# Performance work log

Measured on AMD Instinct MI355X. Metric: run time of the kernel, lower is better.

The kernel has to match this reference:

```python
import math
import jax, jax.numpy as jnp
import numpy as np

H, D_H = 16, 128  # heads, head_dim; d = H*D_H = 2048

def _heads_view(w, rank):
    # w: (d, r) -> (H, r, d_h), matching torch view(H, d_h, r).transpose(1, 2)
    return jnp.transpose(w.reshape(H, D_H, rank), (0, 2, 1))

def setup_inputs() -> dict:
    key = jax.random.key(0)
    ks = jax.random.split(key, 9)
    d, rq, rk, rv = 2048, 512, 512, 512
    B, T = 2, 2048
    s = 0.02  # GPT-2 style init scale keeps logits numerically sane
    return {
        "x": jax.random.normal(ks[0], (B, T, d), dtype=jnp.float32),
        "q_down_w": jax.random.normal(ks[1], (rq, d), dtype=jnp.float32) * s,
        "k_down_w": jax.random.normal(ks[2], (rk, d), dtype=jnp.float32) * s,
        "v_down_w": jax.random.normal(ks[3], (rv, d), dtype=jnp.float32) * s,
        "q_up_w": jax.random.normal(ks[4], (d, rq), dtype=jnp.float32) * s,
        "k_up_w": jax.random.normal(ks[5], (d, rk), dtype=jnp.float32) * s,
        "v_up_w": jax.random.normal(ks[6], (d, rv), dtype=jnp.float32) * s,
        "out_w": jax.random.normal(ks[7], (d, d), dtype=jnp.float32) * s,
        "out_b": jnp.zeros((d,), dtype=jnp.float32),
    }

def reference(x, q_down_w, k_down_w, v_down_w, q_up_w, k_up_w, v_up_w, out_w, out_b):
    B, T, d = x.shape
    rq, rk, rv = q_down_w.shape[0], k_down_w.shape[0], v_down_w.shape[0]
    # Down projections (nn.Linear: x @ W^T)
    Qd = x @ q_down_w.T            # [B, T, rq]
    Kd = x @ k_down_w.T            # [B, S, rk] (S == T, no past_kv)
    Vd = x @ v_down_w.T            # [B, S, rv]
    S = Kd.shape[1]
    # Absorbed score matrix M: [H, rq, rk]
    Uq_h = _heads_view(q_up_w, rq)  # [H, rq, d_h]
    Uk_h = _heads_view(k_up_w, rk)  # [H, rk, d_h]
    M = jnp.einsum('hqd,hkd->hqk', Uq_h, Uk_h) * (1.0 / math.sqrt(D_H))
    # Logits via factorized path: [B,H,T,rk] then [B,H,T,S]
    Qm = jnp.einsum('btq,hqk->bhtk', Qd, M)
    logits = jnp.einsum('bhtk,bsk->bhts', Qm, Kd)
    # Causal mask (P = S - T = 0)
    P = S - T
    i = jnp.arange(T)[:, None]
    j = jnp.arange(S)[None, :]
    future = j > (P + i)
    logits = jnp.where(future[None, None], -jnp.inf, logits)
    attn = jax.nn.softmax(logits.astype(jnp.float32), axis=-1)
    attn = jnp.nan_to_num(attn).astype(x.dtype)
    # Values path
    Uv_h = _heads_view(v_up_w, rv)                      # [H, rv, d_h]
    V_up = jnp.einsum('bsr,hrd->bhsd', Vd, Uv_h)        # [B, H, S, d_h]
    ctx = jnp.einsum('bhts,bhsd->bhtd', attn, V_up)     # [B, H, T, d_h]
    ctx = jnp.transpose(ctx, (0, 2, 1, 3)).reshape(B, T, d)
    out = ctx @ out_w.T + out_b
    return out
```

## Files before the change

### kernel.cpp

```cpp
#include <hip/hip_runtime.h>
#include <stdint.h>

typedef __bf16 bf16x8 __attribute__((ext_vector_type(8)));
typedef float  f32x4  __attribute__((ext_vector_type(4)));
typedef float  f32x16 __attribute__((ext_vector_type(16)));
typedef unsigned short u16;
typedef unsigned int u32;
typedef u16 u16x8 __attribute__((ext_vector_type(8)));
typedef u32 u32x4 __attribute__((ext_vector_type(4)));

__device__ __forceinline__ u16 f2bf(float f) {
  uint32_t u = __builtin_bit_cast(uint32_t, f);
  u += 0x7fffu + ((u >> 16) & 1u);
  return (u16)(u >> 16);
}
__device__ __forceinline__ u32 pack2(float lo, float hi) {
  return (u32)f2bf(lo) | ((u32)f2bf(hi) << 16);
}

__device__ __forceinline__ void async_cp16(const void* src, void* lds) {
  __builtin_amdgcn_global_load_lds(
      (const __attribute__((address_space(1))) uint32_t*)src,
      (__attribute__((address_space(3))) uint32_t*)lds, 16, 0, 0);
}

struct CvtArgs {
  const float* in[8];
  u16* out[8];
  int n8[8];
  int nblk[8];
};
__global__ void cvt_multi(CvtArgs a) {
  int bx = blockIdx.x;
  int t = 0;
  while (t < 7 && bx >= a.nblk[t]) { bx -= a.nblk[t]; ++t; }
  const int i = bx * 256 + threadIdx.x;
  if (i >= a.n8[t]) return;
  const float4* p = (const float4*)a.in[t] + (size_t)i * 2;
  float4 va = p[0], vb = p[1];
  u16x8 r;
  r[0] = f2bf(va.x); r[1] = f2bf(va.y); r[2] = f2bf(va.z); r[3] = f2bf(va.w);
  r[4] = f2bf(vb.x); r[5] = f2bf(vb.y); r[6] = f2bf(vb.z); r[7] = f2bf(vb.w);
  ((u16x8*)a.out[t])[i] = r;
}

struct GemmB3 {
  const u16* A[3];
  const u16* Bm[3];
  u16* C[3];
  float alpha[3];
};

template<bool F32OUT>
__global__ __launch_bounds__(256, 2)
void gemm_bt(GemmB3 args, float* __restrict__ Cf, const float* __restrict__ bias,
             int M, int N, int K)
{
  __shared__ u16 At[128 * 32];
  __shared__ u16 Bt[128 * 32];
  const int z = blockIdx.z;
  const u16* __restrict__ A  = args.A[z];
  const u16* __restrict__ Bw = args.Bm[z];
  const int bm = blockIdx.x * 128;
  const int bn = blockIdx.y * 128;
  const int tid = threadIdx.x;
  const int w  = tid >> 6;
  const int l  = tid & 63;
  const int lr = l & 15;
  const int lg = l >> 4;
  const int wr = (w >> 1) * 64;
  const int wc = (w & 1) * 64;

  f32x4 acc[4][4];
  #pragma unroll
  for (int m = 0; m < 4; ++m)
    #pragma unroll
    for (int n = 0; n < 4; ++n) acc[m][n] = (f32x4){0.f, 0.f, 0.f, 0.f};

  for (int k0 = 0; k0 < K; k0 += 32) {
    __syncthreads();
    #pragma unroll
    for (int i = 0; i < 2; ++i) {
      const int gidx = i * 256 + tid;
      const int row  = gidx >> 2;
      const int g    = gidx & 3;
      const int gs   = (g - (row >> 1)) & 3;
      async_cp16(A  + (size_t)(bm + row) * K + k0 + gs * 8,
                 At + (size_t)(i * 256 + w * 64) * 8);
      async_cp16(Bw + (size_t)(bn + row) * K + k0 + gs * 8,
                 Bt + (size_t)(i * 256 + w * 64) * 8);
    }
    __syncthreads();
    bf16x8 af[4], bfr[4];
    #pragma unroll
    for (int m = 0; m < 4; ++m) {
      const int row = wr + m * 16 + lr;
      const int pos = (lg + (row >> 1)) & 3;
      af[m] = *(const bf16x8*)(At + row * 32 + pos * 8);
    }
    #pragma unroll
    for (int n = 0; n < 4; ++n) {
      const int row = wc + n * 16 + lr;
      const int pos = (lg + (row >> 1)) & 3;
      bfr[n] = *(const bf16x8*)(Bt + row * 32 + pos * 8);
    }
    #pragma unroll
    for (int m = 0; m < 4; ++m)
      #pragma unroll
      for (int n = 0; n < 4; ++n)
        acc[m][n] = __builtin_amdgcn_mfma_f32_16x16x32_bf16(af[m], bfr[n], acc[m][n], 0, 0, 0);
  }

  if constexpr (F32OUT) {
    #pragma unroll
    for (int n = 0; n < 4; ++n) {
      const int col = bn + wc + n * 16 + lr;
      const float bv = bias[col];
      #pragma unroll
      for (int m = 0; m < 4; ++m) {
        const int rbase = bm + wr + m * 16 + lg * 4;
        #pragma unroll
        for (int j = 0; j < 4; ++j)
          Cf[(size_t)(rbase + j) * N + col] = acc[m][n][j] + bv;
      }
    }
  } else {
    u16* __restrict__ C = args.C[z];
    const float alpha = args.alpha[z];
    #pragma unroll
    for (int n = 0; n < 4; ++n) {
      const int col = bn + wc + n * 16 + lr;
      #pragma unroll
      for (int m = 0; m < 4; ++m) {
        const int rbase = bm + wr + m * 16 + lg * 4;
        #pragma unroll
        for (int j = 0; j < 4; ++j)
          C[(size_t)(rbase + j) * N + col] = f2bf(acc[m][n][j] * alpha);
      }
    }
  }
}

__global__ __launch_bounds__(256, 2)
void mla_attn(const u16* __restrict__ Qu, const u16* __restrict__ Ku,
              const u16* __restrict__ Vtg, u16* __restrict__ ctx)
{
  __shared__ u16 Ktb[2][64 * 128];
  __shared__ u16 Vtb[2][128 * 64];

  const int bid = blockIdx.x;
  const int kk  = bid >> 5;
  const int qt  = (kk & 1) ? (kk >> 1) : (15 - (kk >> 1));
  const int bh  = bid & 31;
  const int b = bh >> 4, h = bh & 15;
  const int qbase = qt * 128;
  const int tid = threadIdx.x;
  const int w = tid >> 6, l = tid & 63;
  const int ql = l & 31;
  const int hi = l >> 5;
  const bool hb = (hi != 0);
  const int T = 2048;
  const size_t rs = 2048;

  const u16* Qp = Qu + ((size_t)b * T) * rs + (size_t)h * 128;
  const u16* Kp = Ku + ((size_t)b * T) * rs + (size_t)h * 128;
  const u16* Vp = Vtg + (size_t)(h * 128) * 4096 + (size_t)b * T;

  const int qw = qbase + w * 32;
  const int qg = qw + ql;

  bf16x8 qf[8];
  #pragma unroll
  for (int kb = 0; kb < 8; ++kb)
    qf[kb] = *(const bf16x8*)(Qp + (size_t)qg * rs + kb * 16 + hi * 8);

  f32x16 acc[4];
  #pragma unroll
  for (int dt = 0; dt < 4; ++dt)
    #pragma unroll
    for (int r = 0; r < 16; ++r) acc[dt][r] = 0.f;
  float mrun = -1.0e30f, lsum = 0.f;

  const int ksr = tid >> 4;
  const u16* kb0 = Kp + (size_t)ksr * rs + (((tid & 15) ^ (ksr & 15)) * 8);
  const int vsr = tid >> 3;
  const u16* vb0 = Vp + (size_t)vsr * 4096 + (((tid & 7) ^ (vsr & 7)) * 8);

  const int nT = 2 * qt + 2;

  auto stage = [&](int buf, int it) {
    const int s0 = it * 64;
    #pragma unroll
    for (int i = 0; i < 4; ++i)
      async_cp16(kb0 + (size_t)(s0 + i * 16) * rs, &Ktb[buf][(i * 256 + w * 64) * 8]);
    #pragma unroll
    for (int i = 0; i < 4; ++i)
      async_cp16(vb0 + (size_t)(i * 32) * 4096 + s0, &Vtb[buf][(i * 256 + w * 64) * 8]);
  };

  stage(0, 0);
  int cur = 0;

  for (int it = 0; it < nT; ++it) {
    __syncthreads();
    if (it + 1 < nT) stage(cur ^ 1, it + 1);
    const int s0 = it * 64;
    if (s0 <= qw + 31) {
      const u16* Kt = Ktb[cur];
      const u16* Vt = Vtb[cur];
      const bool diag = (it == (qw >> 6));
      #pragma unroll
      for (int st = 0; st < 2; ++st) {
        f32x16 c;
        #pragma unroll
        for (int r = 0; r < 16; ++r) c[r] = 0.f;
        __builtin_amdgcn_s_setprio(1);
        #pragma unroll
        for (int kb = 0; kb < 8; ++kb) {
          bf16x8 kf = *(const bf16x8*)(Kt + (st * 32 + ql) * 128 +
                                       (((2 * kb + hi) ^ (ql & 15)) * 8));
          c = __builtin_amdgcn_mfma_f32_32x32x16_bf16(kf, qf[kb], c, 0, 0, 0);
        }
        __builtin_amdgcn_s_setprio(0);

        float p[16];
        if (diag) {
          #pragma unroll
          for (int r = 0; r < 16; ++r) {
            const int sgl = s0 + st * 32 + 4 * hi + (r & 3) + 8 * (r >> 2);
            p[r] = (sgl <= qg) ? c[r] : -INFINITY;
          }
        } else {
          #pragma unroll
          for (int r = 0; r < 16; ++r) p[r] = c[r];
        }
        float mx = p[0];
        #pragma unroll
        for (int r = 1; r < 16; ++r) mx = fmaxf(mx, p[r]);
        mx = fmaxf(mx, __shfl_xor(mx, 32));
        if (__any(mx > mrun + 8.f)) {
          const float mnew = fmaxf(mrun, mx);
          const float scl = exp2f(mrun - mnew);
          mrun = mnew;
          lsum *= scl;
          #pragma unroll
          for (int dt = 0; dt < 4; ++dt)
            #pragma unroll
            for (int r = 0; r < 16; ++r) acc[dt][r] *= scl;
        }
        float psum = 0.f;
        #pragma unroll
        for (int r = 0; r < 16; ++r) { p[r] = exp2f(p[r] - mrun); psum += p[r]; }
        lsum += psum + __shfl_xor(psum, 32);

        u32 P0 = pack2(p[0], p[1]),   P1 = pack2(p[2], p[3]);
        u32 P2 = pack2(p[4], p[5]),   P3 = pack2(p[6], p[7]);
        u32 P4 = pack2(p[8], p[9]),   P5 = pack2(p[10], p[11]);
        u32 P6 = pack2(p[12], p[13]), P7 = pack2(p[14], p[15]);
        u32 X0 = __shfl_xor(P0, 32), X1 = __shfl_xor(P1, 32);
        u32 X2 = __shfl_xor(P2, 32), X3 = __shfl_xor(P3, 32);
        u32 X4 = __shfl_xor(P4, 32), X5 = __shfl_xor(P5, 32);
        u32 X6 = __shfl_xor(P6, 32), X7 = __shfl_xor(P7, 32);
        const bf16x8 f0 = __builtin_bit_cast(bf16x8,
            (u32x4){hb ? X2 : P0, hb ? X3 : P1, hb ? P2 : X0, hb ? P3 : X1});
        const bf16x8 f1 = __builtin_bit_cast(bf16x8,
            (u32x4){hb ? X6 : P4, hb ? X7 : P5, hb ? P6 : X4, hb ? P7 : X5});

        __builtin_amdgcn_s_setprio(1);
        #pragma unroll
        for (int dt = 0; dt < 4; ++dt) {
          const int vrow = (dt * 32 + ql) * 64;
          bf16x8 v0 = *(const bf16x8*)(Vt + vrow + (((2 * (2 * st)     + hi) ^ (ql & 7)) * 8));
          bf16x8 v1 = *(const bf16x8*)(Vt + vrow + (((2 * (2 * st + 1) + hi) ^ (ql & 7)) * 8));
          acc[dt] = __builtin_amdgcn_mfma_f32_32x32x16_bf16(v0, f0, acc[dt], 0, 0, 0);
          acc[dt] = __builtin_amdgcn_mfma_f32_32x32x16_bf16(v1, f1, acc[dt], 0, 0, 0);
        }
        __builtin_amdgcn_s_setprio(0);
      }
    }
    cur ^= 1;
  }

  __syncthreads();
  u16* Ot = &Ktb[0][0];
  const float inv = 1.f / lsum;
  const int orow = w * 32 + ql;
  #pragma unroll
  for (int dt = 0; dt < 4; ++dt) {
    #pragma unroll
    for (int rq = 0; rq < 4; ++rq) {
      const int dhb = dt * 32 + 8 * rq + 4 * hi;
      const int dhs = dhb ^ ((ql & 15) << 3);
      u16 e0 = f2bf(acc[dt][rq * 4 + 0] * inv);
      u16 e1 = f2bf(acc[dt][rq * 4 + 1] * inv);
      u16 e2 = f2bf(acc[dt][rq * 4 + 2] * inv);
      u16 e3 = f2bf(acc[dt][rq * 4 + 3] * inv);
      u32 w0 = (u32)e0 | ((u32)e1 << 16);
      u32 w1 = (u32)e2 | ((u32)e3 << 16);
      *(u32*)(Ot + orow * 128 + dhs)     = w0;
      *(u32*)(Ot + orow * 128 + dhs + 2) = w1;
    }
  }
  __syncthreads();
  #pragma unroll
  for (int i = 0; i < 8; ++i) {
    const int n = i * 256 + tid;
    const int q = n >> 4, g = n & 15;
    bf16x8 v = *(const bf16x8*)(Ot + q * 128 + ((g ^ (q & 15)) * 8));
    *(bf16x8*)(ctx + ((size_t)b * T + qbase + q) * rs + h * 128 + g * 8) = v;
  }
}

extern "C" void kernel_launch(void* const* d_in, const int* in_sizes, int n_in,
                              void* d_out, int out_size, void* d_ws, size_t ws_size,
                              hipStream_t stream)
{
  (void)n_in; (void)out_size; (void)ws_size;
  const float* x   = (const float*)d_in[0];
  const float* qdw = (const float*)d_in[1];
  const float* kdw = (const float*)d_in[2];
  const float* vdw = (const float*)d_in[3];
  const float* quw = (const float*)d_in[4];
  const float* kuw = (const float*)d_in[5];
  const float* vuw = (const float*)d_in[6];
  const float* oww = (const float*)d_in[7];
  const float* ob  = (const float*)d_in[8];

  const int d = 2048, r = 512;
  const int BT = in_sizes[0] / d;

  u16* p = (u16*)d_ws;
  auto take = [&](size_t n) { u16* q = p; p += n; return q; };
  u16* xb  = take((size_t)BT * d);
  u16* wqd = take((size_t)r * d);
  u16* wkd = take((size_t)r * d);
  u16* wvd = take((size_t)r * d);
  u16* wqu = take((size_t)d * r);
  u16* wku = take((size_t)d * r);
  u16* wvu = take((size_t)d * r);
  u16* wow = take((size_t)d * d);
  u16* Qd  = take((size_t)BT * r);
  u16* Kd  = take((size_t)BT * r);
  u16* Vd  = take((size_t)BT * r);
  u16* Qu  = take((size_t)BT * d);
  u16* Ku  = take((size_t)BT * d);
  u16* Vtg = take((size_t)BT * d);
  u16* ctx = take((size_t)BT * d);

  CvtArgs ca;
  const float* ins[8] = {x, oww, qdw, kdw, vdw, quw, kuw, vuw};
  u16* outs[8]        = {xb, wow, wqd, wkd, wvd, wqu, wku, wvu};
  const size_t ns[8]  = {(size_t)BT * d, (size_t)d * d,
                         (size_t)r * d, (size_t)r * d, (size_t)r * d,
                         (size_t)d * r, (size_t)d * r, (size_t)d * r};
  int total_blk = 0;
  for (int t = 0; t < 8; ++t) {
    ca.in[t] = ins[t]; ca.out[t] = outs[t];
    ca.n8[t] = (int)(ns[t] / 8);
    ca.nblk[t] = (ca.n8[t] + 255) / 256;
    total_blk += ca.nblk[t];
  }
  cvt_multi<<<dim3(total_blk), dim3(256), 0, stream>>>(ca);

  GemmB3 g1;
  g1.A[0] = xb;  g1.A[1] = xb;  g1.A[2] = xb;
  g1.Bm[0] = wqd; g1.Bm[1] = wkd; g1.Bm[2] = wvd;
  g1.C[0] = Qd;  g1.C[1] = Kd;  g1.C[2] = Vd;
  g1.alpha[0] = 1.f; g1.alpha[1] = 1.f; g1.alpha[2] = 1.f;
  gemm_bt<false><<<dim3(BT / 128, r / 128, 3), dim3(256), 0, stream>>>(
      g1, nullptr, nullptr, BT, r, d);

  GemmB3 g2;
  g2.A[0] = Qd;  g2.A[1] = Kd;  g2.A[2] = Kd;
  g2.Bm[0] = wqu; g2.Bm[1] = wku; g2.Bm[2] = wku;
  g2.C[0] = Qu;  g2.C[1] = Ku;  g2.C[2] = Ku;
  g2.alpha[0] = 0.12751743f; g2.alpha[1] = 1.f; g2.alpha[2] = 1.f;
  gemm_bt<false><<<dim3(BT / 128, d / 128, 2), dim3(256), 0, stream>>>(
      g2, nullptr, nullptr, BT, d, r);

  GemmB3 g2v;
  g2v.A[0] = wvu; g2v.A[1] = wvu; g2v.A[2] = wvu;
  g2v.Bm[0] = Vd; g2v.Bm[1] = Vd; g2v.Bm[2] = Vd;
  g2v.C[0] = Vtg; g2v.C[1] = Vtg; g2v.C[2] = Vtg;
  g2v.alpha[0] = 1.f; g2v.alpha[1] = 1.f; g2v.alpha[2] = 1.f;
  gemm_bt<false><<<dim3(d / 128, BT / 128, 1), dim3(256), 0, stream>>>(
      g2v, nullptr, nullptr, d, BT, r);

  mla_attn<<<dim3(512), dim3(256), 0, stream>>>(Qu, Ku, Vtg, ctx);

  GemmB3 g3;
  g3.A[0] = ctx; g3.A[1] = ctx; g3.A[2] = ctx;
  g3.Bm[0] = wow; g3.Bm[1] = wow; g3.Bm[2] = wow;
  g3.C[0] = nullptr; g3.C[1] = nullptr; g3.C[2] = nullptr;
  g3.alpha[0] = 1.f; g3.alpha[1] = 1.f; g3.alpha[2] = 1.f;
  gemm_bt<true><<<dim3(BT / 128, d / 128, 1), dim3(256), 0, stream>>>(
      g3, (float*)d_out, ob, BT, d, d);
}
```

Before: 239.1 us.

## Widen GEMM K-tile, merge attention sub-tiles, use hardware bf16 pack

The GEMM kernel now stages a 64-wide K slice per barrier pair instead of 32, using an XOR swizzle over 8 groups, which halves the number of sync points. The attention inner loop computes both 32-key score blocks before running a single softmax over all 64 keys, so the max, rescale and sum steps run once per tile instead of twice. Packing to bf16 now uses the v_cvt_pk_bf16_f32 instruction instead of manual rounding. The cross-half exchange is cut from 8 shuffles per sub-tile to 4 by selecting the needed word before the shuffle. The cost is more LDS per GEMM block and more live registers in the attention loop.

```diff
diff --git a/kernel.cpp b/kernel.cpp
--- a/kernel.cpp
+++ b/kernel.cpp
@@ -14,8 +14,10 @@
   u += 0x7fffu + ((u >> 16) & 1u);
   return (u16)(u >> 16);
 }
-__device__ __forceinline__ u32 pack2(float lo, float hi) {
-  return (u32)f2bf(lo) | ((u32)f2bf(hi) << 16);
+__device__ __forceinline__ u32 cvtpk(float lo, float hi) {
+  u32 r;
+  asm("v_cvt_pk_bf16_f32 %0, %1, %2" : "=v"(r) : "v"(lo), "v"(hi));
+  return r;
 }
 
 __device__ __forceinline__ void async_cp16(const void* src, void* lds) {
@@ -56,8 +58,8 @@
 void gemm_bt(GemmB3 args, float* __restrict__ Cf, const float* __restrict__ bias,
              int M, int N, int K)
 {
-  __shared__ u16 At[128 * 32];
-  __shared__ u16 Bt[128 * 32];
+  __shared__ u16 At[128 * 64];
+  __shared__ u16 Bt[128 * 64];
   const int z = blockIdx.z;
   const u16* __restrict__ A  = args.A[z];
   const u16* __restrict__ Bw = args.Bm[z];
@@ -77,38 +79,41 @@
     #pragma unroll
     for (int n = 0; n < 4; ++n) acc[m][n] = (f32x4){0.f, 0.f, 0.f, 0.f};
 
-  for (int k0 = 0; k0 < K; k0 += 32) {
+  for (int k0 = 0; k0 < K; k0 += 64) {
     __syncthreads();
     #pragma unroll
-    for (int i = 0; i < 2; ++i) {
-      const int gidx = i * 256 + tid;
-      const int row  = gidx >> 2;
-      const int g    = gidx & 3;
-      const int gs   = (g - (row >> 1)) & 3;
+    for (int i = 0; i < 4; ++i) {
+      const int slot = i * 256 + tid;
+      const int row  = slot >> 3;
+      const int pos  = slot & 7;
+      const int gs   = pos ^ (row & 7);
       async_cp16(A  + (size_t)(bm + row) * K + k0 + gs * 8,
                  At + (size_t)(i * 256 + w * 64) * 8);
       async_cp16(Bw + (size_t)(bn + row) * K + k0 + gs * 8,
                  Bt + (size_t)(i * 256 + w * 64) * 8);
     }
     __syncthreads();
-    bf16x8 af[4], bfr[4];
-    #pragma unroll
-    for (int m = 0; m < 4; ++m) {
-      const int row = wr + m * 16 + lr;
-      const int pos = (lg + (row >> 1)) & 3;
-      af[m] = *(const bf16x8*)(At + row * 32 + pos * 8);
-    }
-    #pragma unroll
-    for (int n = 0; n < 4; ++n) {
-      const int row = wc + n * 16 + lr;
-      const int pos = (lg + (row >> 1)) & 3;
-      bfr[n] = *(const bf16x8*)(Bt + row * 32 + pos * 8);
-    }
-    #pragma unroll
-    for (int m = 0; m < 4; ++m)
-      #pragma unroll
-      for (int n = 0; n < 4; ++n)
-        acc[m][n] = __builtin_amdgcn_mfma_f32_16x16x32_bf16(af[m], bfr[n], acc[m][n], 0, 0, 0);
+    #pragma unroll
+    for (int kk = 0; kk < 2; ++kk) {
+      bf16x8 af[4], bfr[4];
+      #pragma unroll
+      for (int m = 0; m < 4; ++m) {
+        const int row = wr + m * 16 + lr;
+        const int pos = (kk * 4 + lg) ^ (row & 7);
+        af[m] = *(const bf16x8*)(At + row * 64 + pos * 8);
+      }
+      #pragma unroll
+      for (int n = 0; n < 4; ++n) {
+        const int row = wc + n * 16 + lr;
+        const int pos = (kk * 4 + lg) ^ (row & 7);
+        bfr[n] = *(const bf16x8*)(Bt + row * 64 + pos * 8);
+      }
+      #pragma unroll
+      for (int m = 0; m < 4; ++m)
+        #pragma unroll
+        for (int n = 0; n < 4; ++n)
+          acc[m][n] = __builtin_amdgcn_mfma_f32_16x16x32_bf16(af[m], bfr[n], acc[m][n], 0, 0, 0);
+    }
   }
 
   if constexpr (F32OUT) {
@@ -209,74 +214,83 @@
       const u16* Kt = Ktb[cur];
       const u16* Vt = Vtb[cur];
       const bool diag = (it == (qw >> 6));
+
+      f32x16 c0, c1;
+      #pragma unroll
+      for (int r = 0; r < 16; ++r) { c0[r] = 0.f; c1[r] = 0.f; }
+      __builtin_amdgcn_s_setprio(1);
+      #pragma unroll
+      for (int kb = 0; kb < 8; ++kb) {
+        bf16x8 kf0 = *(const bf16x8*)(Kt + ql * 128 + (((2 * kb + hi) ^ (ql & 15)) * 8));
+        c0 = __builtin_amdgcn_mfma_f32_32x32x16_bf16(kf0, qf[kb], c0, 0, 0, 0);
+      }
+      #pragma unroll
+      for (int kb = 0; kb < 8; ++kb) {
+        bf16x8 kf1 = *(const bf16x8*)(Kt + (32 + ql) * 128 + (((2 * kb + hi) ^ (ql & 15)) * 8));
+        c1 = __builtin_amdgcn_mfma_f32_32x32x16_bf16(kf1, qf[kb], c1, 0, 0, 0);
+      }
+      __builtin_amdgcn_s_setprio(0);
+
+      float p[32];
+      if (diag) {
+        #pragma unroll
+        for (int r = 0; r < 16; ++r) {
+          const int sg0 = s0 + 4 * hi + (r & 3) + 8 * (r >> 2);
+          p[r]      = (sg0      <= qg) ? c0[r] : -INFINITY;
+          p[16 + r] = (sg0 + 32 <= qg) ? c1[r] : -INFINITY;
+        }
+      } else {
+        #pragma unroll
+        for (int r = 0; r < 16; ++r) { p[r] = c0[r]; p[16 + r] = c1[r]; }
+      }
+      float mx = fmaxf(p[0], p[1]);
+      #pragma unroll
+      for (int r = 2; r < 32; ++r) mx = fmaxf(mx, p[r]);
+      mx = fmaxf(mx, __shfl_xor(mx, 32));
+      if (__any(mx > mrun + 8.f)) {
+        const float mnew = fmaxf(mrun, mx);
+        const float scl = exp2f(mrun - mnew);
+        mrun = mnew;
+        lsum *= scl;
+        #pragma unroll
+        for (int dt = 0; dt < 4; ++dt)
+          #pragma unroll
+          for (int r = 0; r < 16; ++r) acc[dt][r] *= scl;
+      }
+      float psum = 0.f;
+      #pragma unroll
+      for (int r = 0; r < 32; ++r) { p[r] = exp2f(p[r] - mrun); psum += p[r]; }
+      lsum += psum + __shfl_xor(psum, 32);
+
+      bf16x8 fr[4];
       #pragma unroll
       for (int st = 0; st < 2; ++st) {
-        f32x16 c;
-        #pragma unroll
-        for (int r = 0; r < 16; ++r) c[r] = 0.f;
-        __builtin_amdgcn_s_setprio(1);
-        #pragma unroll
-        for (int kb = 0; kb < 8; ++kb) {
-          bf16x8 kf = *(const bf16x8*)(Kt + (st * 32 + ql) * 128 +
-                                       (((2 * kb + hi) ^ (ql & 15)) * 8));
-          c = __builtin_amdgcn_mfma_f32_32x32x16_bf16(kf, qf[kb], c, 0, 0, 0);
+        const int o = st * 16;
+        u32 P0 = cvtpk(p[o + 0], p[o + 1]),   P1 = cvtpk(p[o + 2], p[o + 3]);
+        u32 P2 = cvtpk(p[o + 4], p[o + 5]),   P3 = cvtpk(p[o + 6], p[o + 7]);
+        u32 P4 = cvtpk(p[o + 8], p[o + 9]),   P5 = cvtpk(p[o + 10], p[o + 11]);
+        u32 P6 = cvtpk(p[o + 12], p[o + 13]), P7 = cvtpk(p[o + 14], p[o + 15]);
+        u32 Y0 = __shfl_xor(hb ? P0 : P2, 32);
+        u32 Y1 = __shfl_xor(hb ? P1 : P3, 32);
+        u32 Y2 = __shfl_xor(hb ? P4 : P6, 32);
+        u32 Y3 = __shfl_xor(hb ? P5 : P7, 32);
+        fr[st * 2 + 0] = __builtin_bit_cast(bf16x8,
+            (u32x4){hb ? Y0 : P0, hb ? Y1 : P1, hb ? P2 : Y0, hb ? P3 : Y1});
+        fr[st * 2 + 1] = __builtin_bit_cast(bf16x8,
+            (u32x4){hb ? Y2 : P4, hb ? Y3 : P5, hb ? P6 : Y2, hb ? P7 : Y3});
+      }
+
+      __builtin_amdgcn_s_setprio(1);
+      #pragma unroll
+      for (int dt = 0; dt < 4; ++dt) {
+        const int vrow = (dt * 32 + ql) * 64;
+        #pragma unroll
+        for (int ks = 0; ks < 4; ++ks) {
+          bf16x8 v = *(const bf16x8*)(Vt + vrow + (((2 * ks + hi) ^ (ql & 7)) * 8));
+          acc[dt] = __builtin_amdgcn_mfma_f32_32x32x16_bf16(v, fr[ks], acc[dt], 0, 0, 0);
         }
-        __builtin_amdgcn_s_setprio(0);
-
-        float p[16];
-        if (diag) {
-          #pragma unroll
-          for (int r = 0; r < 16; ++r) {
-            const int sgl = s0 + st * 32 + 4 * hi + (r & 3) + 8 * (r >> 2);
-            p[r] = (sgl <= qg) ? c[r] : -INFINITY;
-          }
-        } else {
-          #pragma unroll
-          for (int r = 0; r < 16; ++r) p[r] = c[r];
-        }
-        float mx = p[0];
-        #pragma unroll
-        for (int r = 1; r < 16; ++r) mx = fmaxf(mx, p[r]);
-        mx = fmaxf(mx, __shfl_xor(mx, 32));
-        if (__any(mx > mrun + 8.f)) {
-          const float mnew = fmaxf(mrun, mx);
-          const float scl = exp2f(mrun - mnew);
-          mrun = mnew;
-          lsum *= scl;
-          #pragma unroll
-          for (int dt = 0; dt < 4; ++dt)
-            #pragma unroll
-            for (int r = 0; r < 16; ++r) acc[dt][r] *= scl;
-        }
-        float psum = 0.f;
-        #pragma unroll
-        for (int r = 0; r < 16; ++r) { p[r] = exp2f(p[r] - mrun); psum += p[r]; }
-        lsum += psum + __shfl_xor(psum, 32);
-
-        u32 P0 = pack2(p[0], p[1]),   P1 = pack2(p[2], p[3]);
-        u32 P2 = pack2(p[4], p[5]),   P3 = pack2(p[6], p[7]);
-        u32 P4 = pack2(p[8], p[9]),   P5 = pack2(p[10], p[11]);
-        u32 P6 = pack2(p[12], p[13]), P7 = pack2(p[14], p[15]);
-        u32 X0 = __shfl_xor(P0, 32), X1 = __shfl_xor(P1, 32);
-        u32 X2 = __shfl_xor(P2, 32), X3 = __shfl_xor(P3, 32);
-        u32 X4 = __shfl_xor(P4, 32), X5 = __shfl_xor(P5, 32);
-        u32 X6 = __shfl_xor(P6, 32), X7 = __shfl_xor(P7, 32);
-        const bf16x8 f0 = __builtin_bit_cast(bf16x8,
-            (u32x4){hb ? X2 : P0, hb ? X3 : P1, hb ? P2 : X0, hb ? P3 : X1});
-        const bf16x8 f1 = __builtin_bit_cast(bf16x8,
-            (u32x4){hb ? X6 : P4, hb ? X7 : P5, hb ? P6 : X4, hb ? P7 : X5});
-
-        __builtin_amdgcn_s_setprio(1);
-        #pragma unroll
-        for (int dt = 0; dt < 4; ++dt) {
-          const int vrow = (dt * 32 + ql) * 64;
-          bf16x8 v0 = *(const bf16x8*)(Vt + vrow + (((2 * (2 * st)     + hi) ^ (ql & 7)) * 8));
-          bf16x8 v1 = *(const bf16x8*)(Vt + vrow + (((2 * (2 * st + 1) + hi) ^ (ql & 7)) * 8));
-          acc[dt] = __builtin_amdgcn_mfma_f32_32x32x16_bf16(v0, f0, acc[dt], 0, 0, 0);
-          acc[dt] = __builtin_amdgcn_mfma_f32_32x32x16_bf16(v1, f1, acc[dt], 0, 0, 0);
-        }
-        __builtin_amdgcn_s_setprio(0);
-      }
+      }
+      __builtin_amdgcn_s_setprio(0);
     }
     cur ^= 1;
   }
```

Result: faster. 224.7 us (-6.0%).
